# Kernel tuning notes

Measured on AMD Instinct MI355X. Metric: run time of the kernel, lower is better.

## Reference

```python
import jax, jax.numpy as jnp
import numpy as np

EPS = 1e-6


def _feature_map(x):
    # elu(x) + 1
    return jax.nn.elu(x) + 1.0


def _causal_dot(Qb, Kb, V):
    """Causal linear attention numerator for 3 stacked branches.
    Qb, Kb: [3, N, L, H, D]; V: [N, L, H, Dv] -> out [3, N, L, H, Dv].
    out[b,n,l,h,:] = sum_{s<=l} (Qb[b,n,l,h,:] . Kb[b,n,s,h,:]) V[n,s,h,:]
    computed with an O(L) recurrent scan over cumulative KV outer products.
    """
    Qs = jnp.moveaxis(Qb, 2, 0)  # [L, 3, N, H, D]
    Ks = jnp.moveaxis(Kb, 2, 0)  # [L, 3, N, H, D]
    Vs = jnp.moveaxis(V, 1, 0)   # [L, N, H, Dv]
    B, N, _, H, D = Qb.shape
    Dv = V.shape[-1]
    S0 = jnp.zeros((B, N, H, D, Dv), dtype=Qb.dtype)

    def step(S, inp):
        q, k, v = inp  # q,k: [3,N,H,D], v: [N,H,Dv]
        S = S + k[..., :, None] * v[None, :, :, None, :]
        o = jnp.einsum('bnhi,bnhij->bnhj', q, S)
        return S, o

    _, out = jax.lax.scan(step, S0, (Qs, Ks, Vs))  # out: [L,3,N,H,Dv]
    return jnp.moveaxis(out, 0, 2)  # [3,N,L,H,Dv]


def setup_inputs() -> dict:
    key = jax.random.key(0)
    ks = jax.random.split(key, 5)
    N, L, H, D = 4, 2048, 8, 128
    return {
        'queries': jax.random.normal(ks[0], (N, L, H, D), dtype=jnp.float32),
        'q2': jax.random.normal(ks[1], (N, L, H, D), dtype=jnp.float32),
        'keys': jax.random.normal(ks[2], (N, L, H, D), dtype=jnp.float32),
        'values': jax.random.normal(ks[3], (N, L, H, D), dtype=jnp.float32),
        'key_lengths': jnp.ones((N, L), dtype=jnp.float32),
        'omega': jax.random.normal(ks[4], (H, D, D), dtype=jnp.float32),
    }


def reference(queries, q2, keys, values, key_lengths, omega):
    N, L, H, D = queries.shape
    Q = _feature_map(queries)                       # [N,L,H,D]
    K = _feature_map(keys) * key_lengths[:, :, None, None]

    # Delta[n,l,h,i] = l/L for all n,h,i -> projection through omega reduces to
    # (l/L) * sum_i omega[h,i,j], same math as einsum('nlhi,hij->nlhj', Delta, omega).
    delta = (jnp.arange(L, dtype=queries.dtype) / L)        # [L]
    t = delta[:, None, None] * jnp.sum(omega, axis=1)[None]  # [L,H,D]
    sin_t, cos_t = jnp.sin(t), jnp.cos(t)
    s2, c2, sc = sin_t ** 2, cos_t ** 2, sin_t * cos_t       # [L,H,D] each

    # Q_term = sin(phi(q2))^2 * feature_map(queries)
    q2_proj = jnp.einsum('nlhi,hij->nlhj', q2, omega)
    Q_term = (jnp.sin(q2_proj) ** 2) * Q                     # [N,L,H,D]

    # Branch trig weights: Q gets [sin^2, cos^2, sin*cos], K gets [cos^2, sin^2, sin*cos]
    wq = jnp.stack([s2, c2, sc])[:, None]  # [3,1,L,H,D]
    wk = jnp.stack([c2, s2, sc])[:, None]
    Qb = Q_term[None] * wq                 # [3,N,L,H,D]
    Kb = K[None] * wk                      # [3,N,L,H,D]

    # Denominator terms Z_b = <Q_b[l], cumsum_{s<=l} K_b[s]>
    Kcum = jnp.cumsum(Kb, axis=2)
    Z = jnp.einsum('bnlhi,bnlhi->bnlh', Qb, Kcum)   # [3,N,L,H]

    Vb = _causal_dot(Qb, Kb, values)                # [3,N,L,H,D]

    numerator = Vb[0] + Vb[1] - 2.0 * Vb[2]
    denominator = Z[0] + Z[1] - 2.0 * Z[2] + EPS
    return numerator / denominator[:, :, :, None]
```

## Files before the change

kernel.cpp:

```cpp
#include <hip/hip_runtime.h>


typedef float f32x4 __attribute__((ext_vector_type(4)));
typedef short s16x8 __attribute__((ext_vector_type(8)));
typedef short s16x4 __attribute__((ext_vector_type(4)));
typedef unsigned short u16;

static constexpr int    Ln   = 2048;
static constexpr size_t NHLD = (size_t)32 * 2048 * 128;
static constexpr size_t KSB  = (size_t)32 * 16 * 128;

__device__ __forceinline__ float b2f(u16 s) {
  union { unsigned u; float f; } x; x.u = ((unsigned)s) << 16; return x.f;
}
__device__ __forceinline__ u16 f2b(float f) {
  union { float f; unsigned u; } x; x.f = f;
  unsigned r = x.u + 0x7fffu + ((x.u >> 16) & 1u);
  return (u16)(r >> 16);
}
__device__ __forceinline__ s16x8 pack8(f32x4 a, f32x4 b) {
  s16x8 r;
  r[0] = (short)f2b(a[0]); r[1] = (short)f2b(a[1]); r[2] = (short)f2b(a[2]); r[3] = (short)f2b(a[3]);
  r[4] = (short)f2b(b[0]); r[5] = (short)f2b(b[1]); r[6] = (short)f2b(b[2]); r[7] = (short)f2b(b[3]);
  return r;
}

__global__ __launch_bounds__(256) void k_omega(const float* __restrict__ om,
                                               u16* __restrict__ wt, float* __restrict__ osum) {
  __shared__ alignas(16) u16 T[128][136];
  int h = blockIdx.x, t = threadIdx.x;
  for (int idx = t; idx < 128 * 32; idx += 256) {
    int i = idx >> 5, cs = (idx & 31) << 2;
    f32x4 vv = *(const f32x4*)(om + ((size_t)(h * 128 + i)) * 128 + cs);
    T[i][cs + 0] = f2b(vv[0]); T[i][cs + 1] = f2b(vv[1]);
    T[i][cs + 2] = f2b(vv[2]); T[i][cs + 3] = f2b(vv[3]);
  }
  if (t < 128) {
    float acc = 0.f;
    for (int i = 0; i < 128; i++) acc += om[((size_t)(h * 128 + i)) * 128 + t];
    osum[h * 128 + t] = acc;
  }
  __syncthreads();
  {
    int j = t >> 1, lh = (t & 1) << 6;
    s16x8* dst = (s16x8*)(wt + ((size_t)(h * 128 + j)) * 128 + lh);
    for (int u = 0; u < 8; u++) {
      s16x8 pv;
#pragma unroll
      for (int e = 0; e < 8; e++) pv[e] = (short)T[lh + u * 8 + e][j];
      dst[u] = pv;
    }
  }
}

__global__ __launch_bounds__(512) void k_kvs(const float* __restrict__ kg, const float* __restrict__ vg,
                                             const float* __restrict__ klg, const float* __restrict__ osum,
                                             u16* __restrict__ kb3, u16* __restrict__ vt,
                                             u16* __restrict__ sct, float* __restrict__ ksum) {
  __shared__ union {
    alignas(16) u16 VT[128][128];
    alignas(16) u16 KT[128][136];
  } sm;
  int bid = blockIdx.x, t = threadIdx.x;
  int c = bid & 15, h = (bid >> 4) & 7, n = bid >> 7;
  int l0 = c << 7, nh = (n << 3) + h;
  const float invL = 1.0f / 2048.0f;
  int gcol = t & 31, cs = gcol << 2;
  f32x4 osv = *(const f32x4*)(osum + h * 128 + cs);
#pragma unroll
  for (int it = 0; it < 8; it++) {
    int rr = (it << 4) + (t >> 5);
    int l = l0 + rr;
    size_t gb = (((size_t)(n * Ln + l) * 8 + h) << 7) + cs;
    f32x4 kv = *(const f32x4*)(kg + gb);
    f32x4 vv = *(const f32x4*)(vg + gb);
    float klv = klg[n * Ln + l];
    float tb = (float)l * invL;
    u16 r0[4], r1[4], r2[4];
#pragma unroll
    for (int e = 0; e < 4; e++) {
      float kf = (kv[e] > 0.f ? kv[e] + 1.f : __expf(kv[e])) * klv;
      float tt = tb * osv[e];
      float s, cc; __sincosf(tt, &s, &cc);
      r0[e] = f2b(kf * cc * cc);
      r1[e] = f2b(kf * s * s);
      r2[e] = f2b(kf * s * cc);
    }
    int gs = (gcol ^ (rr >> 3)) << 2;
    *(s16x4*)&sm.VT[rr][gs] = (s16x4){(short)f2b(vv[0]), (short)f2b(vv[1]),
                                      (short)f2b(vv[2]), (short)f2b(vv[3])};
    size_t nb = ((size_t)nh * Ln + l) * 128 + cs;
    *(s16x4*)(kb3 + nb)          = (s16x4){(short)r0[0], (short)r0[1], (short)r0[2], (short)r0[3]};
    *(s16x4*)(kb3 + NHLD + nb)   = (s16x4){(short)r1[0], (short)r1[1], (short)r1[2], (short)r1[3]};
    *(s16x4*)(kb3 + 2*NHLD + nb) = (s16x4){(short)r2[0], (short)r2[1], (short)r2[2], (short)r2[3]};
  }
  __syncthreads();
  size_t bv = ((size_t)(nh * 16 + c)) << 14;
  for (int idx = t; idx < 2048; idx += 512) {
    int i = idx >> 4, o = idx & 15;
    int gp = (((i >> 2) ^ o) << 2) + (i & 3);
    s16x8 v1;
#pragma unroll
    for (int u = 0; u < 8; u++) v1[u] = (short)sm.VT[(o << 3) + u][gp];
    *(s16x8*)(vt + bv + (((size_t)i) << 7) + (o << 3)) = v1;
  }
  int lane = t & 63, quad = lane >> 4, nl = lane & 15, w = t >> 6;
  int arow = (w << 4) + nl;
  const u16* vchunk = vt + bv;
  for (int b = 0; b < 3; b++) {
    int bnh = b * 32 + nh;
    const u16* kb = kb3 + (size_t)b * NHLD + ((size_t)nh * Ln + l0) * 128;
    __syncthreads();
    for (int idx = t; idx < 2048; idx += 512) {
      int s = idx >> 4, io = idx & 15;
      s16x8 v = *(const s16x8*)(kb + (((size_t)s) << 7) + (io << 3));
      int cp = s ^ ((io & 7) << 3);
#pragma unroll
      for (int j = 0; j < 8; j++) sm.KT[(io << 3) + j][cp] = (u16)(short)v[j];
    }
    __syncthreads();
    f32x4 z4 = {0.f, 0.f, 0.f, 0.f};
    f32x4 acc[8];
#pragma unroll
    for (int i = 0; i < 8; i++) acc[i] = z4;
    for (int ks = 0; ks < 4; ks++) {
      int k0 = (ks << 5) + (quad << 3);
      s16x8 av = *(const s16x8*)(vchunk + (((size_t)arow) << 7) + k0);
#pragma unroll
      for (int ct = 0; ct < 8; ct++) {
        int r = (ct << 4) + nl;
        int koff = k0 ^ (((r >> 3) & 7) << 3);
        s16x8 bvv = *(const s16x8*)&sm.KT[r][koff];
        acc[ct] = __builtin_amdgcn_mfma_f32_16x16x32_bf16(av, bvv, acc[ct], 0, 0, 0);
      }
    }
    if (t < 128) {
      float s = 0.f;
      int sw = ((t >> 3) & 7) << 3;
#pragma unroll 4
      for (int g = 0; g < 128; g += 8) {
        s16x8 v = *(const s16x8*)&sm.KT[t][g ^ sw];
#pragma unroll
        for (int e = 0; e < 8; e++) s += b2f((u16)v[e]);
      }
      ksum[(size_t)(bnh * 16 + c) * 128 + t] = s;
    }
    __syncthreads();
    {
      int lbase = (w << 4) + (quad << 2);
#pragma unroll
      for (int ct = 0; ct < 8; ct++) {
        int i = (ct << 4) + nl;
#pragma unroll
        for (int r = 0; r < 4; r++) sm.KT[lbase + r][i] = f2b(acc[ct][r]);
      }
    }
    __syncthreads();
    size_t sbase = ((size_t)(bnh * 16 + c)) << 14;
    for (int idx = t; idx < 2048; idx += 512) {
      int jr = idx >> 4, g = (idx & 15) << 3;
      *(s16x8*)(sct + sbase + ((size_t)jr << 7) + g) = *(const s16x8*)&sm.KT[jr][g];
    }
  }
}

__global__ __launch_bounds__(256) void p1k(float* __restrict__ ksum) {
  int m2 = blockIdx.x * 256 + threadIdx.x;
  int i = m2 & 127, bnh = m2 >> 7;
  size_t base = (size_t)bnh * 2048 + i;
  float acc = 0.f;
  for (int c = 0; c < 16; c++) {
    size_t a = base + (size_t)c * 128;
    float v = ksum[a];
    ksum[a] = acc;
    acc += v;
  }
}

__global__ __launch_bounds__(256, 2) void kqm(const float* __restrict__ q2g, const float* __restrict__ qg,
                                              const u16* __restrict__ wt, const float* __restrict__ osum,
                                              const float* __restrict__ kspre,
                                              u16* __restrict__ qb3, float* __restrict__ zintg,
                                              u16* __restrict__ sct) {
  __shared__ alignas(16) u16 B[128][136];
  __shared__ float osb[128];
  int bid = blockIdx.x, t = threadIdx.x;
  if (bid >= 1024) {
    int tid = (bid - 1024) * 256 + t;
    int bnh = tid >> 11, rem = tid & 2047;
    size_t base = ((size_t)bnh << 18) + ((size_t)rem << 3);
    float acc[8] = {0.f, 0.f, 0.f, 0.f, 0.f, 0.f, 0.f, 0.f};
    for (int c = 0; c < 16; c++) {
      size_t a = base + ((size_t)c << 14);
      s16x8 v = *(const s16x8*)(sct + a);
      s16x8 o;
#pragma unroll
      for (int e = 0; e < 8; e++) { o[e] = (short)f2b(acc[e]); acc[e] += b2f((u16)v[e]); }
      *(s16x8*)(sct + a) = o;
    }
    return;
  }
  int m = bid & 31, h = (bid >> 5) & 7, n = bid >> 8;
  int l0 = m << 6, c = m >> 1, nh = (n << 3) + h;
  if (t < 128) osb[t] = osum[h * 128 + t];
  for (int idx = t; idx < 2048; idx += 256) {
    int j = idx >> 4, cs = (idx & 15) << 3;
    *(s16x8*)&B[j][cs] = *(const s16x8*)(wt + ((size_t)(h * 128 + j)) * 128 + cs);
  }
  __syncthreads();
  int lane = t & 63, quad = lane >> 4, nl = lane & 15, w = t >> 6;
  f32x4 z4 = {0.f, 0.f, 0.f, 0.f};
  f32x4 acc[8];
#pragma unroll
  for (int i = 0; i < 8; i++) acc[i] = z4;
  int arow = l0 + (w << 4) + nl;
  for (int ks = 0; ks < 4; ks++) {
    int k0 = (ks << 5) + (quad << 3);
    const float* ap = q2g + (((size_t)(n * Ln + arow) * 8 + h) << 7) + k0;
    s16x8 av = pack8(*(const f32x4*)ap, *(const f32x4*)(ap + 4));
#pragma unroll
    for (int ct = 0; ct < 8; ct++) {
      s16x8 bv = *(const s16x8*)&B[(ct << 4) + nl][k0];
      acc[ct] = __builtin_amdgcn_mfma_f32_16x16x32_bf16(av, bv, acc[ct], 0, 0, 0);
    }
  }
  __syncthreads();
  {
    int lbase = (w << 4) + (quad << 2);
#pragma unroll
    for (int ct = 0; ct < 8; ct++) {
      int j = (ct << 4) + nl;
#pragma unroll
      for (int r = 0; r < 4; r++) {
        float sp = __sinf(acc[ct][r]);
        B[lbase + r][j] = f2b(sp * sp);
      }
    }
  }
  __syncthreads();
  const float invL = 1.0f / 2048.0f;
  for (int idx = t; idx < 1024; idx += 256) {
    int l = idx >> 4, j0 = (idx & 15) << 3, gl = l0 + l;
    s16x8 s2v = *(const s16x8*)&B[l][j0];
    const float* qp = qg + (((size_t)(n * Ln + gl) * 8 + h) << 7) + j0;
    f32x4 qa = *(const f32x4*)qp, qbv = *(const f32x4*)(qp + 4);
    size_t kbb = ((size_t)nh * 16 + c) * 128 + j0;
    f32x4 kp0a = *(const f32x4*)(kspre + kbb),           kp0b = *(const f32x4*)(kspre + kbb + 4);
    f32x4 kp1a = *(const f32x4*)(kspre + kbb + KSB),     kp1b = *(const f32x4*)(kspre + kbb + KSB + 4);
    f32x4 kp2a = *(const f32x4*)(kspre + kbb + 2 * KSB), kp2b = *(const f32x4*)(kspre + kbb + 2 * KSB + 4);
    s16x8 o0, o1, o2;
    float z = 0.f;
    float tb = (float)gl * invL;
#pragma unroll
    for (int e = 0; e < 8; e++) {
      float s2p = b2f((u16)s2v[e]);
      float qv = (e < 4) ? qa[e] : qbv[e - 4];
      float f = qv > 0.f ? qv + 1.f : __expf(qv);
      float Qt = s2p * f;
      float tt = tb * osb[j0 + e];
      float s, cc; __sincosf(tt, &s, &cc);
      float v0 = Qt * s * s, v1 = Qt * cc * cc, v2 = -2.f * Qt * s * cc;
      float k0v = (e < 4) ? kp0a[e] : kp0b[e - 4];
      float k1v = (e < 4) ? kp1a[e] : kp1b[e - 4];
      float k2v = (e < 4) ? kp2a[e] : kp2b[e - 4];
      z += v0 * k0v + v1 * k1v + v2 * k2v;
      o0[e] = (short)f2b(v0); o1[e] = (short)f2b(v1); o2[e] = (short)f2b(v2);
    }
    size_t base = ((size_t)nh * Ln + gl) * 128 + j0;
    *(s16x8*)(qb3 + base)            = o0;
    *(s16x8*)(qb3 + base + NHLD)     = o1;
    *(s16x8*)(qb3 + base + 2 * NHLD) = o2;
    z += __shfl_xor(z, 1); z += __shfl_xor(z, 2);
    z += __shfl_xor(z, 4); z += __shfl_xor(z, 8);
    if (nl == 0) zintg[(size_t)nh * Ln + gl] = z;
  }
}

__global__ __launch_bounds__(512, 4) void p3(const u16* __restrict__ qb3, const u16* __restrict__ kb3,
                                             const u16* __restrict__ vtg, const u16* __restrict__ sct,
                                             const float* __restrict__ zintg, float* __restrict__ outg) {
  __shared__ union {
    struct { alignas(16) u16 T0[128][128]; alignas(16) u16 T1[128][128]; } s;
    alignas(16) float O[128][132];
  } sm;
  int bid = blockIdx.x, t = threadIdx.x;
  int c = bid & 15, h = (bid >> 4) & 7, n = bid >> 7;
  int l0c = c << 7, nh = (n << 3) + h;
  int lane = t & 63, quad = lane >> 4, nl = lane & 15, w = t >> 6;
  f32x4 z4 = {0.f, 0.f, 0.f, 0.f};
  f32x4 accP[8], accO[8];
#pragma unroll
  for (int i = 0; i < 8; i++) { accP[i] = z4; accO[i] = z4; }
  int arow = l0c + (w << 4) + nl;
  for (int b = 0; b < 3; b++) {
    int bnh = b * 32 + nh;
    __syncthreads();
    for (int idx = t; idx < 2048; idx += 512) {
      int s = idx >> 4;
      int co = (((idx & 15) ^ (s & 7)) << 3);
      *(s16x8*)&sm.s.T0[s][co] = *(const s16x8*)(kb3 + (((size_t)bnh * Ln + l0c + s) << 7) + ((idx & 15) << 3));
    }
    size_t sbase = ((size_t)(bnh * 16 + c)) << 14;
    for (int idx = t; idx < 2048; idx += 512) {
      int j = idx >> 4;
      int co = (((idx & 15) ^ (j & 7)) << 3);
      *(s16x8*)&sm.s.T1[j][co] = *(const s16x8*)(sct + sbase + ((size_t)j << 7) + ((idx & 15) << 3));
    }
    s16x8 av[4];
#pragma unroll
    for (int ks = 0; ks < 4; ks++)
      av[ks] = *(const s16x8*)(qb3 + (((size_t)bnh * Ln + arow) << 7) + (ks << 5) + (quad << 3));
    __syncthreads();
    for (int ks = 0; ks < 4; ks++) {
      int k0 = (ks << 5) + (quad << 3);
#pragma unroll
      for (int ct = 0; ct < 8; ct++) {
        int r = (ct << 4) + nl;
        int koff = k0 ^ ((r & 7) << 3);
        s16x8 bv0 = *(const s16x8*)&sm.s.T0[r][koff];
        accP[ct] = __builtin_amdgcn_mfma_f32_16x16x32_bf16(av[ks], bv0, accP[ct], 0, 0, 0);
        s16x8 bv1 = *(const s16x8*)&sm.s.T1[r][koff];
        accO[ct] = __builtin_amdgcn_mfma_f32_16x16x32_bf16(av[ks], bv1, accO[ct], 0, 0, 0);
      }
    }
  }
  __syncthreads();
  float zP[4] = {0.f, 0.f, 0.f, 0.f};
  int lbase = (w << 4) + (quad << 2);
#pragma unroll
  for (int ct = 0; ct < 8; ct++) {
    int ss = (ct << 4) + nl;
#pragma unroll
    for (int r = 0; r < 4; r++) {
      int lr = lbase + r;
      float pv = (ss <= lr) ? accP[ct][r] : 0.f;
      zP[r] += pv;
      sm.s.T0[lr][ss ^ ((lr & 7) << 3)] = f2b(pv);
    }
  }
#pragma unroll
  for (int mteam = 1; mteam <= 8; mteam <<= 1) {
#pragma unroll
    for (int r = 0; r < 4; r++) zP[r] += __shfl_xor(zP[r], mteam);
  }
  size_t vbase = ((size_t)(nh * 16 + c)) << 14;
  for (int idx = t; idx < 2048; idx += 512) {
    int j = idx >> 4;
    int co = (((idx & 15) ^ (j & 7)) << 3);
    *(s16x8*)&sm.s.T1[j][co] = *(const s16x8*)(vtg + vbase + ((size_t)idx << 3));
  }
  float zf[4];
#pragma unroll
  for (int r = 0; r < 4; r++)
    zf[r] = zintg[(size_t)nh * Ln + l0c + lbase + r] + zP[r] + 1e-6f;
  __syncthreads();
  for (int ks = 0; ks < 4; ks++) {
    int k0 = (ks << 5) + (quad << 3);
    int rw = (w << 4) + nl;
    s16x8 pav = *(const s16x8*)&sm.s.T0[rw][k0 ^ ((rw & 7) << 3)];
#pragma unroll
    for (int ct = 0; ct < 8; ct++) {
      int r = (ct << 4) + nl;
      s16x8 vv = *(const s16x8*)&sm.s.T1[r][k0 ^ ((r & 7) << 3)];
      accO[ct] = __builtin_amdgcn_mfma_f32_16x16x32_bf16(pav, vv, accO[ct], 0, 0, 0);
    }
  }
  __syncthreads();
#pragma unroll
  for (int ct = 0; ct < 8; ct++) {
    int j = (ct << 4) + nl;
#pragma unroll
    for (int r = 0; r < 4; r++) sm.O[lbase + r][j] = accO[ct][r] / zf[r];
  }
  __syncthreads();
  for (int idx = t; idx < 4096; idx += 512) {
    int l = idx >> 5, g = (idx & 31) << 2;
    *(f32x4*)(outg + (((size_t)(n * Ln + l0c + l) * 8 + h) << 7) + g) = *(const f32x4*)&sm.O[l][g];
  }
}

extern "C" void kernel_launch(void* const* d_in, const int* in_sizes, int n_in,
                              void* d_out, int out_size, void* d_ws, size_t ws_size,
                              hipStream_t stream) {
  (void)in_sizes; (void)n_in; (void)out_size; (void)ws_size;
  const float* q   = (const float*)d_in[0];
  const float* q2  = (const float*)d_in[1];
  const float* kk  = (const float*)d_in[2];
  const float* vv  = (const float*)d_in[3];
  const float* kl  = (const float*)d_in[4];
  const float* om  = (const float*)d_in[5];
  float* out = (float*)d_out;

  u16* W     = (u16*)d_ws;
  u16* qb3   = W;
  u16* kb3   = W + 3 * NHLD;
  u16* vt    = W + 6 * NHLD;
  u16* sct   = W + 7 * NHLD;
  u16* wt    = W + 10 * NHLD;
  float* ks  = (float*)(W + 10 * NHLD + 131072);
  float* osm = ks + 196608;
  float* zin = osm + 1024;

  k_omega <<<8,    256, 0, stream>>>(om, wt, osm);
  k_kvs   <<<512,  512, 0, stream>>>(kk, vv, kl, osm, kb3, vt, sct, ks);
  p1k     <<<48,   256, 0, stream>>>(ks);
  kqm     <<<1792, 256, 0, stream>>>(q2, q, wt, osm, ks, qb3, zin, sct);
  p3      <<<512,  512, 0, stream>>>(qb3, kb3, vt, sct, zin, out);
}
```

Measured before the change: 266.9 us.

## Move q2 projection GEMM into the K/V stage as extra blocks

The q2·omega MFMA projection and sin² step move out of the kqm kernel and into extra blocks appended to the K/V preprocessing kernel. Results are written as a bf16 buffer in global memory and read back by kqm. The aim is to fill the GPU better by running the projection alongside the K/V work and to lighten kqm, whose LDS footprint and launch bound are reduced. In exchange it adds an extra global round trip of an NHLD-sized bf16 buffer and a larger workspace.

```diff
diff --git a/kernel.cpp b/kernel.cpp
--- a/kernel.cpp
+++ b/kernel.cpp
@@ -53,18 +53,65 @@
   }
 }
 
-__global__ __launch_bounds__(512) void k_kvs(const float* __restrict__ kg, const float* __restrict__ vg,
-                                             const float* __restrict__ klg, const float* __restrict__ osum,
-                                             u16* __restrict__ kb3, u16* __restrict__ vt,
-                                             u16* __restrict__ sct, float* __restrict__ ksum) {
+__global__ __launch_bounds__(512) void kvsp(const float* __restrict__ kg, const float* __restrict__ vg,
+                                            const float* __restrict__ klg, const float* __restrict__ osum,
+                                            u16* __restrict__ kb3, u16* __restrict__ vt,
+                                            u16* __restrict__ sct, float* __restrict__ ksum,
+                                            const float* __restrict__ q2g, const u16* __restrict__ wtg,
+                                            u16* __restrict__ s2g) {
   __shared__ union {
     alignas(16) u16 VT[128][128];
     alignas(16) u16 KT[128][136];
   } sm;
   int bid = blockIdx.x, t = threadIdx.x;
+  int lane = t & 63, quad = lane >> 4, nl = lane & 15, w = t >> 6;
+  const float invL = 1.0f / 2048.0f;
+  if (bid >= 512) {
+    int pb = bid - 512;
+    int m = pb & 15, h = (pb >> 4) & 7, n = pb >> 7;
+    int l0 = m << 7, nh = (n << 3) + h;
+    for (int idx = t; idx < 2048; idx += 512) {
+      int j = idx >> 4, cs = (idx & 15) << 3;
+      *(s16x8*)&sm.KT[j][cs] = *(const s16x8*)(wtg + ((size_t)(h * 128 + j)) * 128 + cs);
+    }
+    __syncthreads();
+    f32x4 z4 = {0.f, 0.f, 0.f, 0.f};
+    f32x4 acc[8];
+#pragma unroll
+    for (int i = 0; i < 8; i++) acc[i] = z4;
+    int arow = l0 + (w << 4) + nl;
+    for (int ks = 0; ks < 4; ks++) {
+      int k0 = (ks << 5) + (quad << 3);
+      const float* ap = q2g + (((size_t)(n * Ln + arow) * 8 + h) << 7) + k0;
+      s16x8 av = pack8(*(const f32x4*)ap, *(const f32x4*)(ap + 4));
+#pragma unroll
+      for (int ct = 0; ct < 8; ct++) {
+        s16x8 bv = *(const s16x8*)&sm.KT[(ct << 4) + nl][k0];
+        acc[ct] = __builtin_amdgcn_mfma_f32_16x16x32_bf16(av, bv, acc[ct], 0, 0, 0);
+      }
+    }
+    __syncthreads();
+    {
+      int lbase = (w << 4) + (quad << 2);
+#pragma unroll
+      for (int ct = 0; ct < 8; ct++) {
+        int j = (ct << 4) + nl;
+#pragma unroll
+        for (int r = 0; r < 4; r++) {
+          float sp = __sinf(acc[ct][r]);
+          sm.KT[lbase + r][j] = f2b(sp * sp);
+        }
+      }
+    }
+    __syncthreads();
+    for (int idx = t; idx < 2048; idx += 512) {
+      int row = idx >> 4, g = (idx & 15) << 3;
+      *(s16x8*)(s2g + ((size_t)(nh * Ln + l0 + row)) * 128 + g) = *(const s16x8*)&sm.KT[row][g];
+    }
+    return;
+  }
   int c = bid & 15, h = (bid >> 4) & 7, n = bid >> 7;
   int l0 = c << 7, nh = (n << 3) + h;
-  const float invL = 1.0f / 2048.0f;
   int gcol = t & 31, cs = gcol << 2;
   f32x4 osv = *(const f32x4*)(osum + h * 128 + cs);
 #pragma unroll
@@ -104,7 +151,6 @@
     for (int u = 0; u < 8; u++) v1[u] = (short)sm.VT[(o << 3) + u][gp];
     *(s16x8*)(vt + bv + (((size_t)i) << 7) + (o << 3)) = v1;
   }
-  int lane = t & 63, quad = lane >> 4, nl = lane & 15, w = t >> 6;
   int arow = (w << 4) + nl;
   const u16* vchunk = vt + bv;
   for (int b = 0; b < 3; b++) {
@@ -177,12 +223,10 @@
   }
 }
 
-__global__ __launch_bounds__(256, 2) void kqm(const float* __restrict__ q2g, const float* __restrict__ qg,
-                                              const u16* __restrict__ wt, const float* __restrict__ osum,
-                                              const float* __restrict__ kspre,
-                                              u16* __restrict__ qb3, float* __restrict__ zintg,
-                                              u16* __restrict__ sct) {
-  __shared__ alignas(16) u16 B[128][136];
+__global__ __launch_bounds__(256) void kqm(const float* __restrict__ qg, const float* __restrict__ osum,
+                                           const float* __restrict__ kspre, const u16* __restrict__ s2g,
+                                           u16* __restrict__ qb3, float* __restrict__ zintg,
+                                           u16* __restrict__ sct) {
   __shared__ float osb[128];
   int bid = blockIdx.x, t = threadIdx.x;
   if (bid >= 1024) {
@@ -202,46 +246,13 @@
   }
   int m = bid & 31, h = (bid >> 5) & 7, n = bid >> 8;
   int l0 = m << 6, c = m >> 1, nh = (n << 3) + h;
+  int nl = t & 15;
   if (t < 128) osb[t] = osum[h * 128 + t];
-  for (int idx = t; idx < 2048; idx += 256) {
-    int j = idx >> 4, cs = (idx & 15) << 3;
-    *(s16x8*)&B[j][cs] = *(const s16x8*)(wt + ((size_t)(h * 128 + j)) * 128 + cs);
-  }
-  __syncthreads();
-  int lane = t & 63, quad = lane >> 4, nl = lane & 15, w = t >> 6;
-  f32x4 z4 = {0.f, 0.f, 0.f, 0.f};
-  f32x4 acc[8];
-#pragma unroll
-  for (int i = 0; i < 8; i++) acc[i] = z4;
-  int arow = l0 + (w << 4) + nl;
-  for (int ks = 0; ks < 4; ks++) {
-    int k0 = (ks << 5) + (quad << 3);
-    const float* ap = q2g + (((size_t)(n * Ln + arow) * 8 + h) << 7) + k0;
-    s16x8 av = pack8(*(const f32x4*)ap, *(const f32x4*)(ap + 4));
-#pragma unroll
-    for (int ct = 0; ct < 8; ct++) {
-      s16x8 bv = *(const s16x8*)&B[(ct << 4) + nl][k0];
-      acc[ct] = __builtin_amdgcn_mfma_f32_16x16x32_bf16(av, bv, acc[ct], 0, 0, 0);
-    }
-  }
-  __syncthreads();
-  {
-    int lbase = (w << 4) + (quad << 2);
-#pragma unroll
-    for (int ct = 0; ct < 8; ct++) {
-      int j = (ct << 4) + nl;
-#pragma unroll
-      for (int r = 0; r < 4; r++) {
-        float sp = __sinf(acc[ct][r]);
-        B[lbase + r][j] = f2b(sp * sp);
-      }
-    }
-  }
   __syncthreads();
   const float invL = 1.0f / 2048.0f;
   for (int idx = t; idx < 1024; idx += 256) {
     int l = idx >> 4, j0 = (idx & 15) << 3, gl = l0 + l;
-    s16x8 s2v = *(const s16x8*)&B[l][j0];
+    s16x8 s2v = *(const s16x8*)(s2g + ((size_t)nh * Ln + gl) * 128 + j0);
     const float* qp = qg + (((size_t)(n * Ln + gl) * 8 + h) << 7) + j0;
     f32x4 qa = *(const f32x4*)qp, qbv = *(const f32x4*)(qp + 4);
     size_t kbb = ((size_t)nh * 16 + c) * 128 + j0;
@@ -396,14 +407,15 @@
   u16* kb3   = W + 3 * NHLD;
   u16* vt    = W + 6 * NHLD;
   u16* sct   = W + 7 * NHLD;
-  u16* wt    = W + 10 * NHLD;
-  float* ks  = (float*)(W + 10 * NHLD + 131072);
+  u16* s2    = W + 10 * NHLD;
+  u16* wt    = W + 11 * NHLD;
+  float* ks  = (float*)(W + 11 * NHLD + 131072);
   float* osm = ks + 196608;
   float* zin = osm + 1024;
 
   k_omega <<<8,    256, 0, stream>>>(om, wt, osm);
-  k_kvs   <<<512,  512, 0, stream>>>(kk, vv, kl, osm, kb3, vt, sct, ks);
+  kvsp    <<<1024, 512, 0, stream>>>(kk, vv, kl, osm, kb3, vt, sct, ks, q2, wt, s2);
   p1k     <<<48,   256, 0, stream>>>(ks);
-  kqm     <<<1792, 256, 0, stream>>>(q2, q, wt, osm, ks, qb3, zin, sct);
+  kqm     <<<1792, 256, 0, stream>>>(q, osm, ks, s2, qb3, zin, sct);
   p3      <<<512,  512, 0, stream>>>(qb3, kb3, vt, sct, zin, out);
 }
```

New measurement: 273.8 us. +2.6%, slower.
